# Optimization experiments

Hardware: AMD Instinct MI355X
Metric: run time of the kernel (lower is better)

The kernel has to match this reference:

```python
import jax, jax.numpy as jnp
import numpy as np

WS = 8  # window_size; N = WS*WS = 64

def _rel_pos_index(ws):
    # identical to the torch buffer construction (meshgrid default 'ij')
    coords = np.stack(np.meshgrid(np.arange(ws), np.arange(ws), indexing='ij'))  # [2, ws, ws]
    cf = coords.reshape(2, -1)                       # [2, N]
    rel = cf[:, :, None] - cf[:, None, :]            # [2, N, N]
    rel = rel.transpose(1, 2, 0).astype(np.int64)    # [N, N, 2]
    rel[:, :, 0] += ws - 1
    rel[:, :, 1] += ws - 1
    rel[:, :, 0] *= 2 * ws - 1
    return jnp.asarray(rel.sum(-1), dtype=jnp.int32)  # [N, N] in [0, (2ws-1)^2)

def setup_inputs():
    key = jax.random.key(0)
    ks = jax.random.split(key, 4)
    B, N, C, H = 2048, WS * WS, 512, 16
    x = jax.random.normal(ks[0], (B, N, C), jnp.float32)
    qkv_w = jax.random.normal(ks[1], (C, 3 * C), jnp.float32) * 0.02
    proj_w = jax.random.normal(ks[2], (C, C), jnp.float32) * 0.02
    proj_b = jnp.zeros((C,), jnp.float32)
    bias_table = jax.random.normal(ks[3], ((2 * WS - 1) ** 2, H), jnp.float32) * 0.02
    rel_index = _rel_pos_index(WS)
    return {"x": x, "qkv_w": qkv_w, "proj_w": proj_w, "proj_b": proj_b,
            "bias_table": bias_table, "rel_index": rel_index}

def reference(x, qkv_w, proj_w, proj_b, bias_table, rel_index):
    B, N, C = x.shape
    H = bias_table.shape[1]
    d = C // H
    scale = d ** -0.5
    qkv = (x @ qkv_w).reshape(B, N, 3, H, d).transpose(2, 0, 3, 1, 4)  # [3,B,H,N,d]
    q, k, v = qkv[0], qkv[1], qkv[2]
    attn = jnp.einsum('bhnd,bhmd->bhnm', q, k) * scale                 # [B,H,N,N]
    bias = bias_table[rel_index.reshape(-1)].reshape(N, N, H).transpose(2, 0, 1)  # [H,N,N]
    attn = jax.nn.softmax(attn + bias[None], axis=-1)
    attn_map = attn  # dropout ratios are 0 / eval mode -> identity
    out = jnp.einsum('bhnm,bhmd->bhnd', attn, v).transpose(0, 2, 1, 3).reshape(B, N, C)
    out = out @ proj_w + proj_b
    return out, attn_map
```

## Files before the change

### kernel.cpp

```cpp
#include <hip/hip_runtime.h>
#include <cstdint>
#include <cstddef>

#define B_WIN   2048
#define N_TOK   64
#define C_DIM   512
#define H_HEADS 16
#define D_HEAD  32
#define K_DIM   512
#define M_ROWS  (B_WIN * 64)


typedef __bf16 bf16x8 __attribute__((ext_vector_type(8)));
typedef float  f32x4  __attribute__((ext_vector_type(4)));
typedef unsigned short u16x8 __attribute__((ext_vector_type(8)));

__device__ __forceinline__ unsigned short f2bf_rn(float f) {
    unsigned u = __float_as_uint(f);
    u += 0x7fffu + ((u >> 16) & 1u);
    return (unsigned short)(u >> 16);
}
__device__ __forceinline__ float bf2f(unsigned short h) {
    return __uint_as_float(((unsigned)h) << 16);
}
__device__ __forceinline__ void gload16(const void* g, void* l) {
    __builtin_amdgcn_global_load_lds(
        (const __attribute__((address_space(1))) void*)g,
        (__attribute__((address_space(3))) void*)l,
        16, 0, 0);
}

__global__ __launch_bounds__(256) void prep_kernel(
    const float* __restrict__ x,
    unsigned short* __restrict__ Xh,
    unsigned short* __restrict__ Xl,
    const float* __restrict__ qkv_w,
    unsigned short* __restrict__ qwTh,
    unsigned short* __restrict__ qwTl,
    const float* __restrict__ bias_table,
    const int* __restrict__ rel_index,
    float* __restrict__ bias_hn)
{
    const int blk = blockIdx.x;
    if (blk < 32768) {
        size_t e8 = ((size_t)blk * 256 + threadIdx.x) * 8;
        const int mb = (int)(e8 >> 16);
        const int w  = (int)(e8 & 65535);
        const int kt = w >> 12;
        const int s  = (w >> 10) & 3;
        const int r  = (w >> 3) & 127;
        const int m  = mb * 128 + r;
        const int k  = kt * 32 + s * 8;
        const float* src = &x[(size_t)m * 512 + k];
        float4 f0 = *reinterpret_cast<const float4*>(src);
        float4 f1 = *reinterpret_cast<const float4*>(src + 4);
        float fv[8] = {f0.x, f0.y, f0.z, f0.w, f1.x, f1.y, f1.z, f1.w};
        u16x8 hi, lo;
#pragma unroll
        for (int j = 0; j < 8; ++j) {
            unsigned short h = f2bf_rn(fv[j]);
            hi[j] = h;
            lo[j] = f2bf_rn(fv[j] - bf2f(h));
        }
        *reinterpret_cast<u16x8*>(&Xh[e8]) = hi;
        *reinterpret_cast<u16x8*>(&Xl[e8]) = lo;
    } else if (blk < 33152) {
        size_t e8 = ((size_t)(blk - 32768) * 256 + threadIdx.x) * 8;
        const int mb = (int)(e8 >> 16);
        const int ww = (int)(e8 & 65535);
        const int kt = ww >> 12;
        const int s  = (ww >> 10) & 3;
        const int r  = (ww >> 3) & 127;
        const int n  = mb * 128 + r;
        const int k  = kt * 32 + s * 8;
        u16x8 hi, lo;
#pragma unroll
        for (int j = 0; j < 8; ++j) {
            float v = qkv_w[(size_t)(k + j) * 1536 + n];
            unsigned short h = f2bf_rn(v);
            hi[j] = h;
            lo[j] = f2bf_rn(v - bf2f(h));
        }
        *reinterpret_cast<u16x8*>(&qwTh[e8]) = hi;
        *reinterpret_cast<u16x8*>(&qwTl[e8]) = lo;
    } else {
        int tid = (blk - 33152) * 256 + threadIdx.x;
        int h  = tid >> 12;
        int ij = tid & 4095;
        bias_hn[tid] = bias_table[rel_index[ij] * H_HEADS + h];
    }
}

__global__ __launch_bounds__(256) void wsplit_kernel(
    const float* __restrict__ w,
    unsigned short* __restrict__ wTh,
    unsigned short* __restrict__ wTl,
    int Ncols)
{
    size_t e8 = ((size_t)blockIdx.x * 256 + threadIdx.x) * 8;
    const int mb = (int)(e8 >> 16);
    const int ww = (int)(e8 & 65535);
    const int kt = ww >> 12;
    const int s  = (ww >> 10) & 3;
    const int r  = (ww >> 3) & 127;
    const int n  = mb * 128 + r;
    const int k  = kt * 32 + s * 8;
    u16x8 hi, lo;
#pragma unroll
    for (int j = 0; j < 8; ++j) {
        float v = w[(size_t)(k + j) * Ncols + n];
        unsigned short h = f2bf_rn(v);
        hi[j] = h;
        lo[j] = f2bf_rn(v - bf2f(h));
    }
    *reinterpret_cast<u16x8*>(&wTh[e8]) = hi;
    *reinterpret_cast<u16x8*>(&wTl[e8]) = lo;
}

template<int NPASS>
__global__ __launch_bounds__(512, 2) void gemm_mfma_kernel(
    const unsigned short* __restrict__ ATh,
    const unsigned short* __restrict__ ATl,
    const unsigned short* __restrict__ BTh,
    const unsigned short* __restrict__ BTl,
    unsigned short* __restrict__ qh,
    unsigned short* __restrict__ kh,
    unsigned short* __restrict__ vh,
    unsigned short* __restrict__ vl,
    const float* __restrict__ bias,
    float* __restrict__ out,
    int Ncols_out,
    int nb_grid)
{
    extern __shared__ __align__(16) unsigned short L[];
    constexpr int AH = 0;
    constexpr int AL = 8192;
    constexpr int BH = (NPASS == 3) ? 16384 : 8192;
    constexpr int BL = (NPASS == 3) ? 24576 : 16384;
    constexpr int STRIDE = (NPASS == 3) ? 32768 : 24576;

    const int t    = threadIdx.x;
    const int lane = t & 63;
    const int wave = t >> 6;
    const int lg   = lane >> 4;
    const int lr   = lane & 15;
    const int wrow = (wave >> 2) * 128;
    const int wcol = (wave & 3) * 64;

    const int lin = blockIdx.x + gridDim.x * blockIdx.y;
    const int nwg = gridDim.x * gridDim.y;
    const int cpx = nwg >> 3;
    const int swz = (lin & 7) * cpx + (lin >> 3);
    const int m0  = (swz / nb_grid) * 256;
    const int n0  = (swz % nb_grid) * 256;
    const int mb0 = m0 >> 7;
    const int nb0 = n0 >> 7;

    f32x4 acc[8][4];
#pragma unroll
    for (int i = 0; i < 8; ++i)
#pragma unroll
        for (int j = 0; j < 4; ++j) acc[i][j] = (f32x4){0.f, 0.f, 0.f, 0.f};

    auto stage = [&](int kt, int bi) {
        const int bufbase = bi * STRIDE;
#pragma unroll
        for (int i = 0; i < 2; ++i) {
            const int c = i * 512 + t;
            const int r = c & 255;
            const int s = c >> 8;
            const size_t gA = (size_t)(mb0 + (r >> 7)) * 65536
                            + (size_t)kt * 4096 + s * 1024 + (r & 127) * 8;
            const size_t gB = (size_t)(nb0 + (r >> 7)) * 65536
                            + (size_t)kt * 4096 + s * 1024 + (r & 127) * 8;
            const int lo = bufbase + s * 2048 + r * 8;
            gload16(&ATh[gA], &L[lo + AH]);
            if constexpr (NPASS == 3) gload16(&ATl[gA], &L[lo + AL]);
            gload16(&BTh[gB], &L[lo + BH]);
            gload16(&BTl[gB], &L[lo + BL]);
        }
    };

    stage(0, 0);
    asm volatile("s_waitcnt vmcnt(0)" ::: "memory");
    __builtin_amdgcn_sched_barrier(0);
    __builtin_amdgcn_s_barrier();
    __builtin_amdgcn_sched_barrier(0);

#pragma unroll 2
    for (int ks = 0; ks < 16; ++ks) {
        const int cur = ks & 1;
        if (ks + 1 < 16) stage(ks + 1, cur ^ 1);
        const int bb = cur * STRIDE;

        bf16x8 bh[4], bl[4];
#pragma unroll
        for (int ni = 0; ni < 4; ++ni) {
            const int off = bb + lg * 2048 + (wcol + ni * 16 + lr) * 8;
            bh[ni] = *reinterpret_cast<const bf16x8*>(&L[off + BH]);
            bl[ni] = *reinterpret_cast<const bf16x8*>(&L[off + BL]);
        }
        __builtin_amdgcn_s_setprio(1);
#pragma unroll
        for (int mi = 0; mi < 8; ++mi) {
            const int aoff = bb + lg * 2048 + (wrow + mi * 16 + lr) * 8;
            bf16x8 ah = *reinterpret_cast<const bf16x8*>(&L[aoff + AH]);
#pragma unroll
            for (int ni = 0; ni < 4; ++ni)
                acc[mi][ni] = __builtin_amdgcn_mfma_f32_16x16x32_bf16(ah, bh[ni], acc[mi][ni], 0, 0, 0);
#pragma unroll
            for (int ni = 0; ni < 4; ++ni)
                acc[mi][ni] = __builtin_amdgcn_mfma_f32_16x16x32_bf16(ah, bl[ni], acc[mi][ni], 0, 0, 0);
            if constexpr (NPASS == 3) {
                bf16x8 al = *reinterpret_cast<const bf16x8*>(&L[aoff + AL]);
#pragma unroll
                for (int ni = 0; ni < 4; ++ni)
                    acc[mi][ni] = __builtin_amdgcn_mfma_f32_16x16x32_bf16(al, bh[ni], acc[mi][ni], 0, 0, 0);
            }
        }
        __builtin_amdgcn_s_setprio(0);

        asm volatile("s_waitcnt vmcnt(0)" ::: "memory");
        __builtin_amdgcn_sched_barrier(0);
        __builtin_amdgcn_s_barrier();
        __builtin_amdgcn_sched_barrier(0);
    }

    if constexpr (NPASS == 3) {
#pragma unroll
        for (int mi = 0; mi < 8; ++mi)
#pragma unroll
            for (int ni = 0; ni < 4; ++ni) {
                const int col  = n0 + wcol + ni * 16 + lr;
                const int tsel = col >> 9;
                const int h    = (col >> 5) & 15;
                const int dd   = col & 31;
#pragma unroll
                for (int reg = 0; reg < 4; ++reg) {
                    const int row = m0 + wrow + mi * 16 + lg * 4 + reg;
                    const int b = row >> 6, n = row & 63;
                    const size_t idx = ((((size_t)b * H_HEADS + h) * 64) + n) * 32 + dd;
                    const float v = acc[mi][ni][reg];
                    unsigned short hh = f2bf_rn(v);
                    if (tsel == 0) {
                        qh[idx] = hh;
                    } else if (tsel == 1) {
                        kh[idx] = hh;
                    } else {
                        vh[idx] = hh;
                        vl[idx] = f2bf_rn(v - bf2f(hh));
                    }
                }
            }
    } else {
#pragma unroll
        for (int mi = 0; mi < 8; ++mi)
#pragma unroll
            for (int ni = 0; ni < 4; ++ni) {
                const int col = n0 + wcol + ni * 16 + lr;
                const float pb = bias[col];
#pragma unroll
                for (int reg = 0; reg < 4; ++reg) {
                    const int row = m0 + wrow + mi * 16 + lg * 4 + reg;
                    out[(size_t)row * Ncols_out + col] = acc[mi][ni][reg] + pb;
                }
            }
    }
}

__global__ __launch_bounds__(256, 4) void attn_kernel(
    const unsigned short* __restrict__ qh,
    const unsigned short* __restrict__ kh,
    const unsigned short* __restrict__ vh,
    const unsigned short* __restrict__ vl,
    const float* __restrict__ bias_hn,
    float* __restrict__ attn_map,
    unsigned short* __restrict__ avh)
{
    __shared__ __align__(16) unsigned short SM[18944];
    constexpr int VTH = 0, VTL = 2304;
    constexpr int QS  = 4608, KS = 7168;
    constexpr int PH  = 9728, PL = 14336;

    const int bhid = blockIdx.x;
    const int b    = bhid >> 4;
    const int h    = bhid & 15;
    const int t    = threadIdx.x;
    const int lane = t & 63;
    const int wv   = t >> 6;
    const int lg   = lane >> 4;
    const int lr   = lane & 15;

    const size_t base = (size_t)bhid * 2048;

    {
        const int r  = t >> 2;
        const int c0 = (t & 3) * 8;
        u16x8 q8 = *reinterpret_cast<const u16x8*>(&qh[base + r * 32 + c0]);
        *reinterpret_cast<u16x8*>(&SM[QS + r * 40 + c0]) = q8;
        u16x8 k8 = *reinterpret_cast<const u16x8*>(&kh[base + r * 32 + c0]);
        *reinterpret_cast<u16x8*>(&SM[KS + r * 40 + c0]) = k8;
        u16x8 vh8 = *reinterpret_cast<const u16x8*>(&vh[base + r * 32 + c0]);
        u16x8 vl8 = *reinterpret_cast<const u16x8*>(&vl[base + r * 32 + c0]);
#pragma unroll
        for (int u = 0; u < 8; ++u) {
            const int d = c0 + u;
            SM[VTH + d * 72 + r] = vh8[u];
            SM[VTL + d * 72 + r] = vl8[u];
        }
    }
    __syncthreads();

    float bias[4][4];
#pragma unroll
    for (int reg = 0; reg < 4; ++reg)
#pragma unroll
        for (int c = 0; c < 4; ++c)
            bias[reg][c] = bias_hn[(h << 12) + ((wv * 16 + lg * 4 + reg) << 6) + c * 16 + lr];

    const int ar = wv * 16 + lr;
    bf16x8 qa = *reinterpret_cast<const bf16x8*>(&SM[QS + ar * 40 + lg * 8]);
    f32x4 S[4];
#pragma unroll
    for (int c = 0; c < 4; ++c) {
        const int br = c * 16 + lr;
        bf16x8 kb = *reinterpret_cast<const bf16x8*>(&SM[KS + br * 40 + lg * 8]);
        f32x4 s = (f32x4){0.f, 0.f, 0.f, 0.f};
        S[c] = __builtin_amdgcn_mfma_f32_16x16x32_bf16(qa, kb, s, 0, 0, 0);
    }

    const float scale = 0.1767766952966369f;
    float p[4][4], mx[4], sm[4];
#pragma unroll
    for (int reg = 0; reg < 4; ++reg) mx[reg] = -1e30f;
#pragma unroll
    for (int reg = 0; reg < 4; ++reg)
#pragma unroll
        for (int c = 0; c < 4; ++c) {
            float s = fmaf(S[c][reg], scale, bias[reg][c]);
            p[reg][c] = s;
            mx[reg] = fmaxf(mx[reg], s);
        }
#pragma unroll
    for (int reg = 0; reg < 4; ++reg) {
        mx[reg] = fmaxf(mx[reg], __shfl_xor(mx[reg], 1));
        mx[reg] = fmaxf(mx[reg], __shfl_xor(mx[reg], 2));
        mx[reg] = fmaxf(mx[reg], __shfl_xor(mx[reg], 4));
        mx[reg] = fmaxf(mx[reg], __shfl_xor(mx[reg], 8));
        sm[reg] = 0.f;
    }
#pragma unroll
    for (int reg = 0; reg < 4; ++reg)
#pragma unroll
        for (int c = 0; c < 4; ++c) {
            float e = __expf(p[reg][c] - mx[reg]);
            p[reg][c] = e;
            sm[reg] += e;
        }
#pragma unroll
    for (int reg = 0; reg < 4; ++reg) {
        sm[reg] += __shfl_xor(sm[reg], 1);
        sm[reg] += __shfl_xor(sm[reg], 2);
        sm[reg] += __shfl_xor(sm[reg], 4);
        sm[reg] += __shfl_xor(sm[reg], 8);
        const float inv = 1.0f / sm[reg];
#pragma unroll
        for (int c = 0; c < 4; ++c) p[reg][c] *= inv;
    }

    const size_t amb = (size_t)bhid * 4096;
#pragma unroll
    for (int reg = 0; reg < 4; ++reg) {
        const int R = wv * 16 + lg * 4 + reg;
#pragma unroll
        for (int c = 0; c < 4; ++c) {
            const int C = c * 16 + lr;
            const float own = p[reg][c];
            attn_map[amb + R * 64 + C] = own;
            const float mate = __shfl_xor(own, 1);
            if (!(lr & 1)) {
                unsigned short h0 = f2bf_rn(own);
                unsigned short l0 = f2bf_rn(own - bf2f(h0));
                unsigned short h1 = f2bf_rn(mate);
                unsigned short l1 = f2bf_rn(mate - bf2f(h1));
                *reinterpret_cast<unsigned*>(&SM[PH + R * 72 + C]) =
                    (unsigned)h0 | ((unsigned)h1 << 16);
                *reinterpret_cast<unsigned*>(&SM[PL + R * 72 + C]) =
                    (unsigned)l0 | ((unsigned)l1 << 16);
            }
        }
    }

    f32x4 O[2];
    O[0] = (f32x4){0.f, 0.f, 0.f, 0.f};
    O[1] = (f32x4){0.f, 0.f, 0.f, 0.f};
#pragma unroll
    for (int kk = 0; kk < 2; ++kk) {
        const int pr = wv * 16 + lr;
        bf16x8 pa_h = *reinterpret_cast<const bf16x8*>(&SM[PH + pr * 72 + kk * 32 + lg * 8]);
        bf16x8 pa_l = *reinterpret_cast<const bf16x8*>(&SM[PL + pr * 72 + kk * 32 + lg * 8]);
#pragma unroll
        for (int n = 0; n < 2; ++n) {
            const int vr = n * 16 + lr;
            bf16x8 vb_h = *reinterpret_cast<const bf16x8*>(&SM[VTH + vr * 72 + kk * 32 + lg * 8]);
            bf16x8 vb_l = *reinterpret_cast<const bf16x8*>(&SM[VTL + vr * 72 + kk * 32 + lg * 8]);
            O[n] = __builtin_amdgcn_mfma_f32_16x16x32_bf16(pa_h, vb_h, O[n], 0, 0, 0);
            O[n] = __builtin_amdgcn_mfma_f32_16x16x32_bf16(pa_h, vb_l, O[n], 0, 0, 0);
            O[n] = __builtin_amdgcn_mfma_f32_16x16x32_bf16(pa_l, vb_h, O[n], 0, 0, 0);
        }
    }

    const int mb = b >> 1;
#pragma unroll
    for (int n = 0; n < 2; ++n)
#pragma unroll
        for (int reg = 0; reg < 4; ++reg) {
            const int R  = wv * 16 + lg * 4 + reg;
            const int d  = n * 16 + lr;
            const int rl = (b & 1) * 64 + R;
            size_t off = (size_t)mb * 65536 + (size_t)h * 4096
                       + (size_t)(d >> 3) * 1024 + (size_t)rl * 8 + (d & 7);
            avh[off] = f2bf_rn(O[n][reg]);
        }
}

extern "C" void kernel_launch(void* const* d_in, const int* in_sizes, int n_in,
                              void* d_out, int out_size, void* d_ws, size_t ws_size,
                              hipStream_t stream) {
    const float* x          = (const float*)d_in[0];
    const float* qkv_w      = (const float*)d_in[1];
    const float* proj_w     = (const float*)d_in[2];
    const float* proj_b     = (const float*)d_in[3];
    const float* bias_table = (const float*)d_in[4];
    const int*   rel_index  = (const int*)d_in[5];

    float* out      = (float*)d_out;
    float* attn_map = (float*)d_out + (size_t)M_ROWS * C_DIM;

    const size_t PLANE = (size_t)B_WIN * H_HEADS * 64 * 32;
    unsigned short* Xh  = (unsigned short*)d_ws;
    unsigned short* Xl  = Xh + (size_t)M_ROWS * 512;
    unsigned short* qhp = Xl + (size_t)M_ROWS * 512;
    unsigned short* khp = qhp + PLANE;
    unsigned short* vhp = khp + PLANE;
    unsigned short* vlp = vhp + PLANE;
    unsigned short* avh = Xh;

    unsigned short* qwTh = (unsigned short*)attn_map;
    unsigned short* qwTl = qwTh + (size_t)1536 * 512;
    unsigned short* pwTh = qhp;
    unsigned short* pwTl = pwTh + (size_t)512 * 512;
    float* bias_hn = out;

    prep_kernel<<<33408, 256, 0, stream>>>(
        x, Xh, Xl, qkv_w, qwTh, qwTl, bias_table, rel_index, bias_hn);
    gemm_mfma_kernel<3><<<dim3(6, 512), 512, 131072, stream>>>(
        Xh, Xl, qwTh, qwTl, qhp, khp, vhp, vlp, nullptr, nullptr, 1536, 6);
    attn_kernel<<<B_WIN * H_HEADS, 256, 0, stream>>>(
        qhp, khp, vhp, vlp, bias_hn, attn_map, avh);
    wsplit_kernel<<<128, 256, 0, stream>>>(proj_w, pwTh, pwTl, 512);
    gemm_mfma_kernel<2><<<dim3(2, 512), 512, 98304, stream>>>(
        avh, nullptr, pwTh, pwTl, nullptr, nullptr, nullptr, nullptr,
        proj_b, out, 512, 2);
}
```

Baseline: 1.055 ms.

## Use 3-pass split-bf16 only for V columns in QKV GEMM, pack epilogue stores

```diff
diff --git a/kernel.cpp b/kernel.cpp
--- a/kernel.cpp
+++ b/kernel.cpp
@@ -117,7 +117,7 @@
     *reinterpret_cast<u16x8*>(&wTl[e8]) = lo;
 }
 
-template<int NPASS>
+template<int MODE>
 __global__ __launch_bounds__(512, 2) void gemm_mfma_kernel(
     const unsigned short* __restrict__ ATh,
     const unsigned short* __restrict__ ATl,
@@ -135,9 +135,9 @@
     extern __shared__ __align__(16) unsigned short L[];
     constexpr int AH = 0;
     constexpr int AL = 8192;
-    constexpr int BH = (NPASS == 3) ? 16384 : 8192;
-    constexpr int BL = (NPASS == 3) ? 24576 : 16384;
-    constexpr int STRIDE = (NPASS == 3) ? 32768 : 24576;
+    constexpr int BH = (MODE == 0) ? 16384 : 8192;
+    constexpr int BL = (MODE == 0) ? 24576 : 16384;
+    constexpr int STRIDE = (MODE == 0) ? 32768 : 24576;
 
     const int t    = threadIdx.x;
     const int lane = t & 63;
@@ -155,6 +155,8 @@
     const int n0  = (swz % nb_grid) * 256;
     const int mb0 = m0 >> 7;
     const int nb0 = n0 >> 7;
+    const int tsel = n0 >> 9;
+    const bool lo3 = (MODE == 0) && (tsel == 2);
 
     f32x4 acc[8][4];
 #pragma unroll
@@ -175,7 +177,7 @@
                             + (size_t)kt * 4096 + s * 1024 + (r & 127) * 8;
             const int lo = bufbase + s * 2048 + r * 8;
             gload16(&ATh[gA], &L[lo + AH]);
-            if constexpr (NPASS == 3) gload16(&ATl[gA], &L[lo + AL]);
+            if (MODE == 0 && lo3) gload16(&ATl[gA], &L[lo + AL]);
             gload16(&BTh[gB], &L[lo + BH]);
             gload16(&BTl[gB], &L[lo + BL]);
         }
@@ -201,21 +203,33 @@
             bl[ni] = *reinterpret_cast<const bf16x8*>(&L[off + BL]);
         }
         __builtin_amdgcn_s_setprio(1);
-#pragma unroll
-        for (int mi = 0; mi < 8; ++mi) {
-            const int aoff = bb + lg * 2048 + (wrow + mi * 16 + lr) * 8;
-            bf16x8 ah = *reinterpret_cast<const bf16x8*>(&L[aoff + AH]);
-#pragma unroll
-            for (int ni = 0; ni < 4; ++ni)
-                acc[mi][ni] = __builtin_amdgcn_mfma_f32_16x16x32_bf16(ah, bh[ni], acc[mi][ni], 0, 0, 0);
-#pragma unroll
-            for (int ni = 0; ni < 4; ++ni)
-                acc[mi][ni] = __builtin_amdgcn_mfma_f32_16x16x32_bf16(ah, bl[ni], acc[mi][ni], 0, 0, 0);
-            if constexpr (NPASS == 3) {
+        if (lo3) {
+#pragma unroll
+            for (int mi = 0; mi < 8; ++mi) {
+                const int aoff = bb + lg * 2048 + (wrow + mi * 16 + lr) * 8;
+                bf16x8 ah = *reinterpret_cast<const bf16x8*>(&L[aoff + AH]);
                 bf16x8 al = *reinterpret_cast<const bf16x8*>(&L[aoff + AL]);
+#pragma unroll
+                for (int ni = 0; ni < 4; ++ni)
+                    acc[mi][ni] = __builtin_amdgcn_mfma_f32_16x16x32_bf16(ah, bh[ni], acc[mi][ni], 0, 0, 0);
+#pragma unroll
+                for (int ni = 0; ni < 4; ++ni)
+                    acc[mi][ni] = __builtin_amdgcn_mfma_f32_16x16x32_bf16(ah, bl[ni], acc[mi][ni], 0, 0, 0);
 #pragma unroll
                 for (int ni = 0; ni < 4; ++ni)
                     acc[mi][ni] = __builtin_amdgcn_mfma_f32_16x16x32_bf16(al, bh[ni], acc[mi][ni], 0, 0, 0);
+            }
+        } else {
+#pragma unroll
+            for (int mi = 0; mi < 8; ++mi) {
+                const int aoff = bb + lg * 2048 + (wrow + mi * 16 + lr) * 8;
+                bf16x8 ah = *reinterpret_cast<const bf16x8*>(&L[aoff + AH]);
+#pragma unroll
+                for (int ni = 0; ni < 4; ++ni)
+                    acc[mi][ni] = __builtin_amdgcn_mfma_f32_16x16x32_bf16(ah, bh[ni], acc[mi][ni], 0, 0, 0);
+#pragma unroll
+                for (int ni = 0; ni < 4; ++ni)
+                    acc[mi][ni] = __builtin_amdgcn_mfma_f32_16x16x32_bf16(ah, bl[ni], acc[mi][ni], 0, 0, 0);
             }
         }
         __builtin_amdgcn_s_setprio(0);
@@ -226,29 +240,33 @@
         __builtin_amdgcn_sched_barrier(0);
     }
 
-    if constexpr (NPASS == 3) {
+    if constexpr (MODE == 0) {
+        unsigned short* dh = (tsel == 0) ? qh : (tsel == 1) ? kh : vh;
 #pragma unroll
         for (int mi = 0; mi < 8; ++mi)
 #pragma unroll
             for (int ni = 0; ni < 4; ++ni) {
-                const int col  = n0 + wcol + ni * 16 + lr;
-                const int tsel = col >> 9;
-                const int h    = (col >> 5) & 15;
-                const int dd   = col & 31;
+                const int col = n0 + wcol + ni * 16 + lr;
+                const int h   = (col >> 5) & 15;
+                const int dd  = col & 31;
 #pragma unroll
                 for (int reg = 0; reg < 4; ++reg) {
                     const int row = m0 + wrow + mi * 16 + lg * 4 + reg;
                     const int b = row >> 6, n = row & 63;
                     const size_t idx = ((((size_t)b * H_HEADS + h) * 64) + n) * 32 + dd;
-                    const float v = acc[mi][ni][reg];
-                    unsigned short hh = f2bf_rn(v);
-                    if (tsel == 0) {
-                        qh[idx] = hh;
-                    } else if (tsel == 1) {
-                        kh[idx] = hh;
-                    } else {
-                        vh[idx] = hh;
-                        vl[idx] = f2bf_rn(v - bf2f(hh));
+                    const float own  = acc[mi][ni][reg];
+                    const float mate = __shfl_xor(own, 1);
+                    if (!(lr & 1)) {
+                        unsigned short h0 = f2bf_rn(own);
+                        unsigned short h1 = f2bf_rn(mate);
+                        *reinterpret_cast<unsigned*>(&dh[idx]) =
+                            (unsigned)h0 | ((unsigned)h1 << 16);
+                        if (tsel == 2) {
+                            unsigned short l0 = f2bf_rn(own  - bf2f(h0));
+                            unsigned short l1 = f2bf_rn(mate - bf2f(h1));
+                            *reinterpret_cast<unsigned*>(&vl[idx]) =
+                                (unsigned)l0 | ((unsigned)l1 << 16);
+                        }
                     }
                 }
             }
@@ -454,12 +472,12 @@
 
     prep_kernel<<<33408, 256, 0, stream>>>(
         x, Xh, Xl, qkv_w, qwTh, qwTl, bias_table, rel_index, bias_hn);
-    gemm_mfma_kernel<3><<<dim3(6, 512), 512, 131072, stream>>>(
+    gemm_mfma_kernel<0><<<dim3(6, 512), 512, 131072, stream>>>(
         Xh, Xl, qwTh, qwTl, qhp, khp, vhp, vlp, nullptr, nullptr, 1536, 6);
     attn_kernel<<<B_WIN * H_HEADS, 256, 0, stream>>>(
         qhp, khp, vhp, vlp, bias_hn, attn_map, avh);
     wsplit_kernel<<<128, 256, 0, stream>>>(proj_w, pwTh, pwTl, 512);
-    gemm_mfma_kernel<2><<<dim3(2, 512), 512, 98304, stream>>>(
+    gemm_mfma_kernel<1><<<dim3(2, 512), 512, 98304, stream>>>(
         avh, nullptr, pwTh, pwTl, nullptr, nullptr, nullptr, nullptr,
         proj_b, out, 512, 2);
 }
```

New measurement: 2.331 ms. +120.9%, slower.
